# Optimization experiments

Measured on AMD Instinct MI355X. Metric: run time of the kernel, lower is better.

Reference implementation:

```python
import jax, jax.numpy as jnp
import numpy as np

BATCH = 4096
DIM = 128
TEMP = 0.5
EPS = 1e-8


def _neg_mask(batch):
    n = 2 * batch
    m = np.ones((n, n), dtype=bool)
    np.fill_diagonal(m, False)
    idx = np.arange(batch)
    m[idx, idx + batch] = False
    m[idx + batch, idx] = False
    return m


def setup_inputs() -> dict:
    key = jax.random.key(0)
    k1, k2 = jax.random.split(key)
    zx = jax.random.normal(k1, (BATCH, DIM), dtype=jnp.float32)
    zy = jax.random.normal(k2, (BATCH, DIM), dtype=jnp.float32)
    return {"zx": zx, "zy": zy}


def reference(zx, zy):
    batch = zx.shape[0]
    n = 2 * batch  # N = 2 * batch_size
    z = jnp.concatenate([zx, zy], axis=0)  # [N, D]
    # cosine similarity = normalized GEMM (avoids O(N^2*D) intermediate)
    norm = jnp.maximum(jnp.linalg.norm(z, axis=1, keepdims=True), EPS)
    zn = z / norm
    sim = (zn @ zn.T) / TEMP  # [N, N]
    # positives: diagonals at offsets +batch and -batch
    sim_xy = jnp.diagonal(sim, offset=batch)
    sim_yx = jnp.diagonal(sim, offset=-batch)
    positives = jnp.concatenate([sim_xy, sim_yx]).reshape(n, 1)  # [N, 1]
    # negatives: mask out diagonal and positive pairs (static boolean mask)
    mask = _neg_mask(batch)
    negatives = sim[mask].reshape(n, n - 2)  # [N, N-2]
    logits = jnp.concatenate([positives, negatives], axis=1)  # [N, N-1]
    # CrossEntropy(labels=0, reduction='sum') / N
    loss = jnp.sum(jax.nn.logsumexp(logits, axis=1) - logits[:, 0]) / n
    return loss
```

## Files before the change

kernel.cpp:

```cpp
#include <hip/hip_runtime.h>
#include <hip/hip_bf16.h>

#define BATCH 4096
#define NROWS 8192
#define DIM   128

typedef __bf16 bf16x8 __attribute__((ext_vector_type(8)));
typedef __bf16 bf16x2 __attribute__((ext_vector_type(2)));
typedef float  f32x4  __attribute__((ext_vector_type(4)));

typedef const __attribute__((address_space(1))) unsigned int* gptr_t;
typedef __attribute__((address_space(3))) unsigned int* lptr_t;

__global__ __launch_bounds__(256) void normalize_kernel(
    const float* __restrict__ zx, const float* __restrict__ zy,
    ushort* __restrict__ zn)
{
  const int tid  = threadIdx.x;
  const int lane = tid & 63;
  const int w    = tid >> 6;
  const int row  = blockIdx.x * 4 + w;
  const float* src = (row < BATCH) ? (zx + (size_t)row * DIM)
                                   : (zy + (size_t)(row - BATCH) * DIM);
  float2 v = ((const float2*)src)[lane];
  float ss = v.x * v.x + v.y * v.y;
#pragma unroll
  for (int off = 1; off < 64; off <<= 1)
    ss += __shfl_xor(ss, off, 64);
  float inv = 1.0f / fmaxf(sqrtf(ss), 1e-8f);
  bf16x2 st;
  st.x = (__bf16)(v.x * inv);
  st.y = (__bf16)(v.y * inv);
  reinterpret_cast<bf16x2*>(zn + (size_t)row * DIM)[lane] = st;
}

__global__ __launch_bounds__(256, 2) void simloss_kernel(
    const ushort* __restrict__ zn, float* __restrict__ S, float* __restrict__ P)
{
  __shared__ ushort Bs[128 * 128];
  const int tid  = threadIdx.x;
  const int lane = tid & 63;
  const int w    = tid >> 6;
  const int wr   = w >> 1, wc = w & 1;
  const int rb    = blockIdx.x;
  const int strip = blockIdx.y;
  const int q    = lane >> 4;
  const int l15  = lane & 15;

  bf16x8 af[4][4];
  {
    const int arow = rb * 128 + wr * 64 + l15;
#pragma unroll
    for (int mi = 0; mi < 4; ++mi)
#pragma unroll
      for (int ks = 0; ks < 4; ++ks) {
        const ushort* ap = zn + (size_t)(arow + mi * 16) * DIM + ks * 32 + q * 8;
        af[mi][ks] = *reinterpret_cast<const bf16x8*>(ap);
      }
  }

  float Srow[4][4];
#pragma unroll
  for (int mi = 0; mi < 4; ++mi)
#pragma unroll
    for (int r = 0; r < 4; ++r) Srow[mi][r] = 0.f;

  const float K1 = 2.8853900817779268f;

  for (int it = 0; it < 8; ++it) {
    const int ct = strip * 8 + it;
    const int C0 = ct * 128;

    __syncthreads();
#pragma unroll
    for (int j = 0; j < 8; ++j) {
      const int Lbase = w * 512 + j * 64;
      const int row   = w * 32 + j * 4 + q;
      const int c     = l15 ^ (row & 15);
      const ushort* g = zn + (size_t)(C0 + row) * DIM + c * 8;
      __builtin_amdgcn_global_load_lds((gptr_t)g, (lptr_t)(Bs + Lbase * 8), 16, 0, 0);
    }
    __syncthreads();

    f32x4 acc[4][4];
#pragma unroll
    for (int mi = 0; mi < 4; ++mi)
#pragma unroll
      for (int ni = 0; ni < 4; ++ni)
        acc[mi][ni] = (f32x4){0.f, 0.f, 0.f, 0.f};

#pragma unroll
    for (int ks = 0; ks < 4; ++ks) {
      bf16x8 bf[4];
#pragma unroll
      for (int ni = 0; ni < 4; ++ni) {
        const int nl  = wc * 64 + ni * 16 + l15;
        const int ck  = ks * 4 + q;
        const int L   = nl * 16 + (ck ^ (nl & 15));
        bf[ni] = *reinterpret_cast<const bf16x8*>(Bs + L * 8);
      }
#pragma unroll
      for (int mi = 0; mi < 4; ++mi)
#pragma unroll
        for (int ni = 0; ni < 4; ++ni)
          acc[mi][ni] = __builtin_amdgcn_mfma_f32_16x16x32_bf16(
              af[mi][ks], bf[ni], acc[mi][ni], 0, 0, 0);
    }

    const bool diag = (ct == rb);
    const bool part = (ct == (rb ^ 32));
#pragma unroll
    for (int mi = 0; mi < 4; ++mi)
#pragma unroll
      for (int ni = 0; ni < 4; ++ni)
#pragma unroll
        for (int r = 0; r < 4; ++r) {
          float d = acc[mi][ni][r];
          float v = __builtin_amdgcn_exp2f(fmaf(d, K1, -K1));
          if (diag) {
            const int rl = wr * 64 + mi * 16 + q * 4 + r;
            const int cl = wc * 64 + ni * 16 + l15;
            if (rl == cl) v = 0.f;
          }
          Srow[mi][r] += v;
        }

    if (part) {
#pragma unroll
      for (int mi = 0; mi < 4; ++mi) {
        const int rl0 = wr * 64 + mi * 16 + q * 4;
#pragma unroll
        for (int ni = 0; ni < 4; ++ni) {
          const int cl = wc * 64 + ni * 16 + l15;
#pragma unroll
          for (int r = 0; r < 4; ++r) {
            if (cl == rl0 + r)
              P[rb * 128 + rl0 + r] = 2.0f * acc[mi][ni][r];
          }
        }
      }
    }
  }

#pragma unroll
  for (int mi = 0; mi < 4; ++mi)
#pragma unroll
    for (int r = 0; r < 4; ++r) {
      float v = Srow[mi][r];
      v += __shfl_xor(v, 1, 64);
      v += __shfl_xor(v, 2, 64);
      v += __shfl_xor(v, 4, 64);
      v += __shfl_xor(v, 8, 64);
      if (l15 == 0)
        atomicAdd(&S[rb * 128 + wr * 64 + mi * 16 + q * 4 + r], v);
    }
}

__global__ __launch_bounds__(256) void finalize_kernel(
    const float* __restrict__ S, const float* __restrict__ P,
    float* __restrict__ out)
{
  const int i = blockIdx.x * 256 + threadIdx.x;
  float c = 2.0f + logf(S[i]) - P[i];
#pragma unroll
  for (int off = 1; off < 64; off <<= 1)
    c += __shfl_xor(c, off, 64);
  __shared__ float wsum[4];
  const int lane = threadIdx.x & 63, w = threadIdx.x >> 6;
  if (lane == 0) wsum[w] = c;
  __syncthreads();
  if (threadIdx.x == 0)
    atomicAdd(out, (wsum[0] + wsum[1] + wsum[2] + wsum[3]) * (1.0f / NROWS));
}

extern "C" void kernel_launch(void* const* d_in, const int* in_sizes, int n_in,
                              void* d_out, int out_size, void* d_ws, size_t ws_size,
                              hipStream_t stream)
{
  const float* zx = (const float*)d_in[0];
  const float* zy = (const float*)d_in[1];
  ushort* zn = (ushort*)d_ws;
  float*  S  = (float*)((char*)d_ws + (size_t)NROWS * DIM * 2);
  float*  P  = S + NROWS;
  float*  out = (float*)d_out;

  hipMemsetAsync(S, 0, NROWS * sizeof(float), stream);
  hipMemsetAsync(out, 0, sizeof(float), stream);
  normalize_kernel<<<NROWS / 4, 256, 0, stream>>>(zx, zy, zn);
  simloss_kernel<<<dim3(64, 8), 256, 0, stream>>>(zn, S, P);
  finalize_kernel<<<NROWS / 256, 256, 0, stream>>>(S, P, out);
}
```

Measured before the change: 88.62 us.

## Exploit symmetry of similarity matrix with triangular tiling and fold memsets into normalize

The similarity matrix is symmetric, so the kernel now computes only the lower-triangular 128x64 tiles (4160 blocks) and adds each tile's exp sums to both the row and the column accumulators. This roughly halves the MFMA and exp work. Positives are written for both partner rows from a single tile. The two memset calls are removed and their zeroing moved into normalize_kernel. In exchange the kernel needs a per-block binary search to map the block index to a tile, more global atomics for the column sums, and smaller tiles with higher occupancy.

```diff
diff --git a/kernel.cpp b/kernel.cpp
--- a/kernel.cpp
+++ b/kernel.cpp
@@ -4,6 +4,8 @@
 #define BATCH 4096
 #define NROWS 8192
 #define DIM   128
+#define NTILE 64
+#define NBLK  4160
 
 typedef __bf16 bf16x8 __attribute__((ext_vector_type(8)));
 typedef __bf16 bf16x2 __attribute__((ext_vector_type(2)));
@@ -14,12 +16,14 @@
 
 __global__ __launch_bounds__(256) void normalize_kernel(
     const float* __restrict__ zx, const float* __restrict__ zy,
-    ushort* __restrict__ zn)
+    ushort* __restrict__ zn, float* __restrict__ S, float* __restrict__ out)
 {
   const int tid  = threadIdx.x;
   const int lane = tid & 63;
   const int w    = tid >> 6;
   const int row  = blockIdx.x * 4 + w;
+  if (blockIdx.x < 32) S[blockIdx.x * 256 + tid] = 0.f;
+  if (blockIdx.x == 0 && tid == 0) out[0] = 0.f;
   const float* src = (row < BATCH) ? (zx + (size_t)row * DIM)
                                    : (zy + (size_t)(row - BATCH) * DIM);
   float2 v = ((const float2*)src)[lane];
@@ -34,24 +38,47 @@
   reinterpret_cast<bf16x2*>(zn + (size_t)row * DIM)[lane] = st;
 }
 
-__global__ __launch_bounds__(256, 2) void simloss_kernel(
-    const ushort* __restrict__ zn, float* __restrict__ S, float* __restrict__ P)
-{
-  __shared__ ushort Bs[128 * 128];
+__global__ __launch_bounds__(256, 4) void simloss_kernel(
+    const ushort* __restrict__ zn, float* __restrict__ S,
+    float* __restrict__ P)
+{
+  __shared__ ushort Bs[64 * 128];
   const int tid  = threadIdx.x;
   const int lane = tid & 63;
   const int w    = tid >> 6;
-  const int wr   = w >> 1, wc = w & 1;
-  const int rb    = blockIdx.x;
-  const int strip = blockIdx.y;
   const int q    = lane >> 4;
   const int l15  = lane & 15;
 
-  bf16x8 af[4][4];
+  const int v = (blockIdx.x & 7) * 520 + (blockIdx.x >> 3);
+
+  int rb;
   {
-    const int arow = rb * 128 + wr * 64 + l15;
-#pragma unroll
-    for (int mi = 0; mi < 4; ++mi)
+    int lo = 0, hi = NTILE - 1;
+    while (lo < hi) {
+      int mid = (lo + hi + 1) >> 1;
+      if (mid * (mid + 1) <= v) lo = mid; else hi = mid - 1;
+    }
+    rb = lo;
+  }
+  const int cp = v - rb * (rb + 1);
+  const int c0 = cp * 64;
+  const bool diag = ((cp >> 1) == rb);
+  const bool pos  = (rb >= 32) && ((cp >> 1) == rb - 32);
+
+#pragma unroll
+  for (int j = 0; j < 4; ++j) {
+    const int Lbase = j * 256 + w * 64;
+    const int row   = j * 16 + w * 4 + q;
+    const int c     = l15 ^ (row & 15);
+    const ushort* g = zn + (size_t)(c0 + row) * DIM + c * 8;
+    __builtin_amdgcn_global_load_lds((gptr_t)g, (lptr_t)(Bs + Lbase * 8), 16, 0, 0);
+  }
+
+  bf16x8 af[2][4];
+  {
+    const int arow = rb * 128 + w * 32 + l15;
+#pragma unroll
+    for (int mi = 0; mi < 2; ++mi)
 #pragma unroll
       for (int ks = 0; ks < 4; ++ks) {
         const ushort* ap = zn + (size_t)(arow + mi * 16) * DIM + ks * 32 + q * 8;
@@ -59,101 +86,88 @@
       }
   }
 
-  float Srow[4][4];
-#pragma unroll
-  for (int mi = 0; mi < 4; ++mi)
-#pragma unroll
-    for (int r = 0; r < 4; ++r) Srow[mi][r] = 0.f;
+  __syncthreads();
+
+  f32x4 acc[2][4];
+#pragma unroll
+  for (int mi = 0; mi < 2; ++mi)
+#pragma unroll
+    for (int ni = 0; ni < 4; ++ni)
+      acc[mi][ni] = (f32x4){0.f, 0.f, 0.f, 0.f};
+
+#pragma unroll
+  for (int ks = 0; ks < 4; ++ks) {
+    bf16x8 bf[4];
+#pragma unroll
+    for (int ni = 0; ni < 4; ++ni) {
+      const int nl = ni * 16 + l15;
+      const int ck = ks * 4 + q;
+      const int L  = nl * 16 + (ck ^ (nl & 15));
+      bf[ni] = *reinterpret_cast<const bf16x8*>(Bs + L * 8);
+    }
+#pragma unroll
+    for (int mi = 0; mi < 2; ++mi)
+#pragma unroll
+      for (int ni = 0; ni < 4; ++ni)
+        acc[mi][ni] = __builtin_amdgcn_mfma_f32_16x16x32_bf16(
+            af[mi][ks], bf[ni], acc[mi][ni], 0, 0, 0);
+  }
 
   const float K1 = 2.8853900817779268f;
-
-  for (int it = 0; it < 8; ++it) {
-    const int ct = strip * 8 + it;
-    const int C0 = ct * 128;
-
-    __syncthreads();
-#pragma unroll
-    for (int j = 0; j < 8; ++j) {
-      const int Lbase = w * 512 + j * 64;
-      const int row   = w * 32 + j * 4 + q;
-      const int c     = l15 ^ (row & 15);
-      const ushort* g = zn + (size_t)(C0 + row) * DIM + c * 8;
-      __builtin_amdgcn_global_load_lds((gptr_t)g, (lptr_t)(Bs + Lbase * 8), 16, 0, 0);
-    }
-    __syncthreads();
-
-    f32x4 acc[4][4];
-#pragma unroll
-    for (int mi = 0; mi < 4; ++mi)
-#pragma unroll
-      for (int ni = 0; ni < 4; ++ni)
-        acc[mi][ni] = (f32x4){0.f, 0.f, 0.f, 0.f};
-
-#pragma unroll
-    for (int ks = 0; ks < 4; ++ks) {
-      bf16x8 bf[4];
-#pragma unroll
-      for (int ni = 0; ni < 4; ++ni) {
-        const int nl  = wc * 64 + ni * 16 + l15;
-        const int ck  = ks * 4 + q;
-        const int L   = nl * 16 + (ck ^ (nl & 15));
-        bf[ni] = *reinterpret_cast<const bf16x8*>(Bs + L * 8);
-      }
-#pragma unroll
-      for (int mi = 0; mi < 4; ++mi)
-#pragma unroll
-        for (int ni = 0; ni < 4; ++ni)
-          acc[mi][ni] = __builtin_amdgcn_mfma_f32_16x16x32_bf16(
-              af[mi][ks], bf[ni], acc[mi][ni], 0, 0, 0);
-    }
-
-    const bool diag = (ct == rb);
-    const bool part = (ct == (rb ^ 32));
-#pragma unroll
-    for (int mi = 0; mi < 4; ++mi)
-#pragma unroll
-      for (int ni = 0; ni < 4; ++ni)
-#pragma unroll
-        for (int r = 0; r < 4; ++r) {
-          float d = acc[mi][ni][r];
-          float v = __builtin_amdgcn_exp2f(fmaf(d, K1, -K1));
-          if (diag) {
-            const int rl = wr * 64 + mi * 16 + q * 4 + r;
-            const int cl = wc * 64 + ni * 16 + l15;
-            if (rl == cl) v = 0.f;
-          }
-          Srow[mi][r] += v;
-        }
-
-    if (part) {
-#pragma unroll
-      for (int mi = 0; mi < 4; ++mi) {
-        const int rl0 = wr * 64 + mi * 16 + q * 4;
-#pragma unroll
-        for (int ni = 0; ni < 4; ++ni) {
-          const int cl = wc * 64 + ni * 16 + l15;
-#pragma unroll
-          for (int r = 0; r < 4; ++r) {
-            if (cl == rl0 + r)
-              P[rb * 128 + rl0 + r] = 2.0f * acc[mi][ni][r];
-          }
+  f32x4 Srow[2];
+  float Scol[4];
+#pragma unroll
+  for (int mi = 0; mi < 2; ++mi) Srow[mi] = (f32x4){0.f, 0.f, 0.f, 0.f};
+#pragma unroll
+  for (int ni = 0; ni < 4; ++ni) Scol[ni] = 0.f;
+
+#pragma unroll
+  for (int mi = 0; mi < 2; ++mi)
+#pragma unroll
+    for (int ni = 0; ni < 4; ++ni) {
+      f32x4 vv;
+#pragma unroll
+      for (int r = 0; r < 4; ++r) {
+        const int rl   = w * 32 + mi * 16 + q * 4 + r;
+        const int grow = rb * 128 + rl;
+        const int gcol = c0 + ni * 16 + l15;
+        float d = acc[mi][ni][r];
+        float val = __builtin_amdgcn_exp2f(fmaf(d, K1, -K1));
+        if (diag && gcol == grow) val = 0.f;
+        vv[r] = val;
+        if (pos && gcol == grow - 4096) {
+          const float pv = 2.0f * d;
+          P[grow] = pv;
+          P[grow - 4096] = pv;
         }
       }
-    }
-  }
-
-#pragma unroll
-  for (int mi = 0; mi < 4; ++mi)
+      Srow[mi] += vv;
+      Scol[ni] += (vv[0] + vv[1]) + (vv[2] + vv[3]);
+    }
+
+#pragma unroll
+  for (int mi = 0; mi < 2; ++mi)
 #pragma unroll
     for (int r = 0; r < 4; ++r) {
-      float v = Srow[mi][r];
-      v += __shfl_xor(v, 1, 64);
-      v += __shfl_xor(v, 2, 64);
-      v += __shfl_xor(v, 4, 64);
-      v += __shfl_xor(v, 8, 64);
+      float s = Srow[mi][r];
+      s += __shfl_xor(s, 1, 64);
+      s += __shfl_xor(s, 2, 64);
+      s += __shfl_xor(s, 4, 64);
+      s += __shfl_xor(s, 8, 64);
       if (l15 == 0)
-        atomicAdd(&S[rb * 128 + wr * 64 + mi * 16 + q * 4 + r], v);
-    }
+        atomicAdd(&S[rb * 128 + w * 32 + mi * 16 + q * 4 + r], s);
+    }
+
+  if (!diag) {
+#pragma unroll
+    for (int ni = 0; ni < 4; ++ni) {
+      float s = Scol[ni];
+      s += __shfl_xor(s, 16, 64);
+      s += __shfl_xor(s, 32, 64);
+      if (lane < 16)
+        atomicAdd(&S[c0 + ni * 16 + l15], s);
+    }
+  }
 }
 
 __global__ __launch_bounds__(256) void finalize_kernel(
@@ -180,13 +194,11 @@
   const float* zx = (const float*)d_in[0];
   const float* zy = (const float*)d_in[1];
   ushort* zn = (ushort*)d_ws;
-  float*  S  = (float*)((char*)d_ws + (size_t)NROWS * DIM * 2);
-  float*  P  = S + NROWS;
+  float*  P  = (float*)((char*)d_ws + (size_t)NROWS * DIM * 2);
+  float*  S  = P + NROWS;
   float*  out = (float*)d_out;
 
-  hipMemsetAsync(S, 0, NROWS * sizeof(float), stream);
-  hipMemsetAsync(out, 0, sizeof(float), stream);
-  normalize_kernel<<<NROWS / 4, 256, 0, stream>>>(zx, zy, zn);
-  simloss_kernel<<<dim3(64, 8), 256, 0, stream>>>(zn, S, P);
+  normalize_kernel<<<NROWS / 4, 256, 0, stream>>>(zx, zy, zn, S, out);
+  simloss_kernel<<<NBLK, 256, 0, stream>>>(zn, S, P);
   finalize_kernel<<<NROWS / 256, 256, 0, stream>>>(S, P, out);
 }
```

Result: slower. 109.0 us (+23.0%).
